# Kernel tuning notes

Hardware: AMD Instinct MI355X
Metric: run time of the kernel (lower is better)

Reference implementation:

```python
import jax, jax.numpy as jnp
import numpy as np

THRESHOLD = 0.01


def setup_inputs() -> dict:
    key = jax.random.key(0)
    kv_cache = jax.random.normal(key, (2, 16, 8192, 128), dtype=jnp.float32)
    return {"kv_cache": kv_cache}


def _dequantize_bin(kv, binmask, levels):
    # min/max restricted to the bin via +-inf sentinels (no dynamic shapes)
    inf = jnp.float32(jnp.inf)
    bmin = jnp.min(jnp.where(binmask, kv, inf))
    bmax = jnp.max(jnp.where(binmask, kv, -inf))
    has_any = jnp.any(binmask)
    valid = has_any & (bmax != bmin)
    denom = jnp.where(valid, bmax - bmin, jnp.float32(1.0))  # safe denom
    q = jnp.round((kv - bmin) / denom * levels)
    deq = q / levels * denom + bmin
    return jnp.where(binmask & valid, deq, kv)


def reference(kv_cache):
    mask = jnp.abs(kv_cache) > THRESHOLD  # large-value bin
    out = _dequantize_bin(kv_cache, ~mask, jnp.float32(15.0))   # small bin: 4-bit
    out = jnp.where(mask, _dequantize_bin(kv_cache, mask, jnp.float32(255.0)), out)  # large bin: 8-bit
    return out
```

## Files before the change

### kernel.cpp

```cpp
#include <hip/hip_runtime.h>

static constexpr float kThresh = 0.01f;
static constexpr int TPB     = 256;
static constexpr int PBLOCKS = 2048;
static constexpr int DBLOCKS = 2048;

__device__ __forceinline__ unsigned fkey(float f) {
    unsigned u = __float_as_uint(f);
    return (u & 0x80000000u) ? ~u : (u | 0x80000000u);
}
__device__ __forceinline__ float unkey(unsigned k) {
    unsigned u = (k & 0x80000000u) ? (k & 0x7fffffffu) : ~k;
    return __uint_as_float(u);
}

__device__ __forceinline__ void acc_one(float x, unsigned& smin, unsigned& smax,
                                        unsigned& lmin, unsigned& lmax) {
    unsigned k = fkey(x);
    if (fabsf(x) > kThresh) {
        lmin = min(lmin, k);
        lmax = max(lmax, k);
    } else {
        smin = min(smin, k);
        smax = max(smax, k);
    }
}

__device__ __forceinline__ void acc4(float4 v, unsigned& smin, unsigned& smax,
                                     unsigned& lmin, unsigned& lmax) {
    acc_one(v.x, smin, smax, lmin, lmax);
    acc_one(v.y, smin, smax, lmin, lmax);
    acc_one(v.z, smin, smax, lmin, lmax);
    acc_one(v.w, smin, smax, lmin, lmax);
}

__device__ __forceinline__ void wave_reduce4(unsigned& smin, unsigned& smax,
                                             unsigned& lmin, unsigned& lmax) {
    #pragma unroll
    for (int off = 32; off > 0; off >>= 1) {
        smin = min(smin, (unsigned)__shfl_down((int)smin, off));
        smax = max(smax, (unsigned)__shfl_down((int)smax, off));
        lmin = min(lmin, (unsigned)__shfl_down((int)lmin, off));
        lmax = max(lmax, (unsigned)__shfl_down((int)lmax, off));
    }
}

__device__ __forceinline__ float deq1(float x, float smin, float ssc, float sis, bool sv,
                                      float lmin, float lsc, float lis, bool lv) {
    bool large = fabsf(x) > kThresh;
    float bmin = large ? lmin : smin;
    float sc   = large ? lsc : ssc;
    float is   = large ? lis : sis;
    bool  v    = large ? lv : sv;
    float q = rintf((x - bmin) * sc);
    float d = fmaf(q, is, bmin);
    return v ? d : x;
}

__global__ __launch_bounds__(TPB) void kv_partial(const float* __restrict__ in, int n,
                                                  unsigned* __restrict__ partials) {
    unsigned smin = 0xFFFFFFFFu, smax = 0u, lmin = 0xFFFFFFFFu, lmax = 0u;
    const int n4 = n >> 2;
    const float4* __restrict__ in4 = (const float4*)in;
    const int stride = gridDim.x * TPB;
    int i = blockIdx.x * TPB + threadIdx.x;
    for (; i + 3 * stride < n4; i += 4 * stride) {
        float4 a = in4[i];
        float4 b = in4[i + stride];
        float4 c = in4[i + 2 * stride];
        float4 d = in4[i + 3 * stride];
        acc4(a, smin, smax, lmin, lmax);
        acc4(b, smin, smax, lmin, lmax);
        acc4(c, smin, smax, lmin, lmax);
        acc4(d, smin, smax, lmin, lmax);
    }
    for (; i < n4; i += stride) acc4(in4[i], smin, smax, lmin, lmax);
    for (int j = (n4 << 2) + blockIdx.x * TPB + threadIdx.x; j < n; j += stride)
        acc_one(in[j], smin, smax, lmin, lmax);

    wave_reduce4(smin, smax, lmin, lmax);

    __shared__ unsigned ls[4][4];
    const int wave = threadIdx.x >> 6;
    if ((threadIdx.x & 63) == 0) {
        ls[wave][0] = smin; ls[wave][1] = smax; ls[wave][2] = lmin; ls[wave][3] = lmax;
    }
    __syncthreads();
    if (threadIdx.x == 0) {
        unsigned a = ls[0][0], b = ls[0][1], c = ls[0][2], d = ls[0][3];
        #pragma unroll
        for (int w = 1; w < 4; ++w) {
            a = min(a, ls[w][0]); b = max(b, ls[w][1]);
            c = min(c, ls[w][2]); d = max(d, ls[w][3]);
        }
        partials[blockIdx.x * 4 + 0] = a;
        partials[blockIdx.x * 4 + 1] = b;
        partials[blockIdx.x * 4 + 2] = c;
        partials[blockIdx.x * 4 + 3] = d;
    }
}

__global__ __launch_bounds__(TPB) void kv_final(const unsigned* __restrict__ partials,
                                                unsigned* __restrict__ ws) {
    unsigned smin = 0xFFFFFFFFu, smax = 0u, lmin = 0xFFFFFFFFu, lmax = 0u;
    for (int i = threadIdx.x; i < PBLOCKS; i += TPB) {
        smin = min(smin, partials[4 * i + 0]);
        smax = max(smax, partials[4 * i + 1]);
        lmin = min(lmin, partials[4 * i + 2]);
        lmax = max(lmax, partials[4 * i + 3]);
    }
    wave_reduce4(smin, smax, lmin, lmax);

    __shared__ unsigned ls[4][4];
    const int wave = threadIdx.x >> 6;
    if ((threadIdx.x & 63) == 0) {
        ls[wave][0] = smin; ls[wave][1] = smax; ls[wave][2] = lmin; ls[wave][3] = lmax;
    }
    __syncthreads();
    if (threadIdx.x == 0) {
        unsigned a = ls[0][0], b = ls[0][1], c = ls[0][2], d = ls[0][3];
        #pragma unroll
        for (int w = 1; w < 4; ++w) {
            a = min(a, ls[w][0]); b = max(b, ls[w][1]);
            c = min(c, ls[w][2]); d = max(d, ls[w][3]);
        }
        ws[0] = a; ws[1] = b; ws[2] = c; ws[3] = d;
    }
}

__global__ __launch_bounds__(TPB) void kv_dequant(const float* __restrict__ in,
                                                  float* __restrict__ out, int n,
                                                  const unsigned* __restrict__ partials,
                                                  int pcount) {
    unsigned fa = 0xFFFFFFFFu, fb = 0u, fc = 0xFFFFFFFFu, fd = 0u;
    for (int p = threadIdx.x; p < pcount; p += TPB) {
        fa = min(fa, partials[4 * p + 0]);
        fb = max(fb, partials[4 * p + 1]);
        fc = min(fc, partials[4 * p + 2]);
        fd = max(fd, partials[4 * p + 3]);
    }
    wave_reduce4(fa, fb, fc, fd);

    __shared__ unsigned ls[4][4];
    __shared__ float sc8[8];
    const int wave = threadIdx.x >> 6;
    if ((threadIdx.x & 63) == 0) {
        ls[wave][0] = fa; ls[wave][1] = fb; ls[wave][2] = fc; ls[wave][3] = fd;
    }
    __syncthreads();
    if (threadIdx.x == 0) {
        unsigned a = ls[0][0], b = ls[0][1], c = ls[0][2], d = ls[0][3];
        #pragma unroll
        for (int w = 1; w < 4; ++w) {
            a = min(a, ls[w][0]); b = max(b, ls[w][1]);
            c = min(c, ls[w][2]); d = max(d, ls[w][3]);
        }
        bool sv = a < b;
        bool lv = c < d;
        float smn  = unkey(a);
        float sden = sv ? (unkey(b) - smn) : 1.0f;
        float lmn  = unkey(c);
        float lden = lv ? (unkey(d) - lmn) : 1.0f;
        sc8[0] = smn; sc8[1] = 15.0f / sden;  sc8[2] = sden / 15.0f;
        sc8[3] = lmn; sc8[4] = 255.0f / lden; sc8[5] = lden / 255.0f;
        sc8[6] = sv ? 1.0f : 0.0f;
        sc8[7] = lv ? 1.0f : 0.0f;
    }
    __syncthreads();
    const float smn = sc8[0], ssc = sc8[1], sis = sc8[2];
    const float lmn = sc8[3], lsc = sc8[4], lis = sc8[5];
    const bool  sv  = sc8[6] != 0.0f, lv = sc8[7] != 0.0f;

    const int n4 = n >> 2;
    const float4* __restrict__ in4 = (const float4*)in;
    float4* __restrict__ out4 = (float4*)out;
    const int stride = gridDim.x * TPB;
    int k = blockIdx.x * TPB + threadIdx.x;
    for (; k + 3 * stride < n4; k += 4 * stride) {
        float4 a = in4[k];
        float4 b = in4[k + stride];
        float4 c = in4[k + 2 * stride];
        float4 d = in4[k + 3 * stride];
        float4 ra, rb, rc, rd;
        ra.x = deq1(a.x, smn, ssc, sis, sv, lmn, lsc, lis, lv);
        ra.y = deq1(a.y, smn, ssc, sis, sv, lmn, lsc, lis, lv);
        ra.z = deq1(a.z, smn, ssc, sis, sv, lmn, lsc, lis, lv);
        ra.w = deq1(a.w, smn, ssc, sis, sv, lmn, lsc, lis, lv);
        rb.x = deq1(b.x, smn, ssc, sis, sv, lmn, lsc, lis, lv);
        rb.y = deq1(b.y, smn, ssc, sis, sv, lmn, lsc, lis, lv);
        rb.z = deq1(b.z, smn, ssc, sis, sv, lmn, lsc, lis, lv);
        rb.w = deq1(b.w, smn, ssc, sis, sv, lmn, lsc, lis, lv);
        rc.x = deq1(c.x, smn, ssc, sis, sv, lmn, lsc, lis, lv);
        rc.y = deq1(c.y, smn, ssc, sis, sv, lmn, lsc, lis, lv);
        rc.z = deq1(c.z, smn, ssc, sis, sv, lmn, lsc, lis, lv);
        rc.w = deq1(c.w, smn, ssc, sis, sv, lmn, lsc, lis, lv);
        rd.x = deq1(d.x, smn, ssc, sis, sv, lmn, lsc, lis, lv);
        rd.y = deq1(d.y, smn, ssc, sis, sv, lmn, lsc, lis, lv);
        rd.z = deq1(d.z, smn, ssc, sis, sv, lmn, lsc, lis, lv);
        rd.w = deq1(d.w, smn, ssc, sis, sv, lmn, lsc, lis, lv);
        out4[k]              = ra;
        out4[k + stride]     = rb;
        out4[k + 2 * stride] = rc;
        out4[k + 3 * stride] = rd;
    }
    for (; k < n4; k += stride) {
        float4 a = in4[k];
        float4 r;
        r.x = deq1(a.x, smn, ssc, sis, sv, lmn, lsc, lis, lv);
        r.y = deq1(a.y, smn, ssc, sis, sv, lmn, lsc, lis, lv);
        r.z = deq1(a.z, smn, ssc, sis, sv, lmn, lsc, lis, lv);
        r.w = deq1(a.w, smn, ssc, sis, sv, lmn, lsc, lis, lv);
        out4[k] = r;
    }
    for (int j = (n4 << 2) + blockIdx.x * TPB + threadIdx.x; j < n; j += stride)
        out[j] = deq1(in[j], smn, ssc, sis, sv, lmn, lsc, lis, lv);
}

extern "C" void kernel_launch(void* const* d_in, const int* in_sizes, int n_in,
                              void* d_out, int out_size, void* d_ws, size_t ws_size,
                              hipStream_t stream) {
    const float* in = (const float*)d_in[0];
    float* out = (float*)d_out;
    unsigned* ws = (unsigned*)d_ws;
    const int n = in_sizes[0];

    if (ws_size >= (size_t)(PBLOCKS * 4) * sizeof(unsigned)) {
        unsigned* pt = ws;
        kv_partial<<<PBLOCKS, TPB, 0, stream>>>(in, n, pt);
        kv_dequant<<<DBLOCKS, TPB, 0, stream>>>(in, out, n, pt, PBLOCKS);
    } else {
        unsigned* pt = (unsigned*)d_out;
        kv_partial<<<PBLOCKS, TPB, 0, stream>>>(in, n, pt);
        kv_final<<<1, TPB, 0, stream>>>(pt, ws);
        kv_dequant<<<DBLOCKS, TPB, 0, stream>>>(in, out, n, ws, 1);
    }
}
```

Measured before the change: 255.6 us.

## Fuse min/max reduction and dequant into one cooperative kernel with grid sync

Replaces the two-kernel pipeline (partial reduction, then dequant that re-reduces partials) with one cooperative kernel. It computes per-block min/max, does a grid-wide sync, reduces the partials once per block and then dequantizes. This removes a kernel launch boundary and shrinks the partial count to 1024 blocks. The cost is a grid barrier, the 1024-block limit on parallelism, and a second full read of the 64MB input that the L2/MALL is unlikely to cache. If the cooperative launch fails, the code falls back to the old path.

```diff
diff --git a/kernel.cpp b/kernel.cpp
--- a/kernel.cpp
+++ b/kernel.cpp
@@ -1,7 +1,11 @@
 #include <hip/hip_runtime.h>
+#include <hip/hip_cooperative_groups.h>
+
+namespace cg = cooperative_groups;
 
 static constexpr float kThresh = 0.01f;
 static constexpr int TPB     = 256;
+static constexpr int NBLK    = 1024;
 static constexpr int PBLOCKS = 2048;
 static constexpr int DBLOCKS = 2048;
 
@@ -55,6 +59,131 @@
     float q = rintf((x - bmin) * sc);
     float d = fmaf(q, is, bmin);
     return v ? d : x;
+}
+
+__global__ __launch_bounds__(TPB, 4) void kv_fused(const float* __restrict__ in,
+                                                   float* __restrict__ out, int n,
+                                                   unsigned* __restrict__ pt) {
+    const int n4 = n >> 2;
+    const float4* __restrict__ in4 = (const float4*)in;
+    const int tid = blockIdx.x * TPB + threadIdx.x;
+    const int stride = NBLK * TPB;
+
+    unsigned smin = 0xFFFFFFFFu, smax = 0u, lmin = 0xFFFFFFFFu, lmax = 0u;
+    int i = tid;
+    for (; i + 3 * stride < n4; i += 4 * stride) {
+        float4 a = in4[i];
+        float4 b = in4[i + stride];
+        float4 c = in4[i + 2 * stride];
+        float4 d = in4[i + 3 * stride];
+        acc4(a, smin, smax, lmin, lmax);
+        acc4(b, smin, smax, lmin, lmax);
+        acc4(c, smin, smax, lmin, lmax);
+        acc4(d, smin, smax, lmin, lmax);
+    }
+    for (; i < n4; i += stride) acc4(in4[i], smin, smax, lmin, lmax);
+    for (int j = (n4 << 2) + tid; j < n; j += stride)
+        acc_one(in[j], smin, smax, lmin, lmax);
+
+    wave_reduce4(smin, smax, lmin, lmax);
+
+    __shared__ unsigned ls[4][4];
+    __shared__ float sc8[8];
+    const int wave = threadIdx.x >> 6;
+    if ((threadIdx.x & 63) == 0) {
+        ls[wave][0] = smin; ls[wave][1] = smax; ls[wave][2] = lmin; ls[wave][3] = lmax;
+    }
+    __syncthreads();
+    if (threadIdx.x == 0) {
+        unsigned a = ls[0][0], b = ls[0][1], c = ls[0][2], d = ls[0][3];
+        #pragma unroll
+        for (int w = 1; w < 4; ++w) {
+            a = min(a, ls[w][0]); b = max(b, ls[w][1]);
+            c = min(c, ls[w][2]); d = max(d, ls[w][3]);
+        }
+        __hip_atomic_store(&pt[blockIdx.x + 0 * NBLK], a, __ATOMIC_RELAXED, __HIP_MEMORY_SCOPE_AGENT);
+        __hip_atomic_store(&pt[blockIdx.x + 1 * NBLK], b, __ATOMIC_RELAXED, __HIP_MEMORY_SCOPE_AGENT);
+        __hip_atomic_store(&pt[blockIdx.x + 2 * NBLK], c, __ATOMIC_RELAXED, __HIP_MEMORY_SCOPE_AGENT);
+        __hip_atomic_store(&pt[blockIdx.x + 3 * NBLK], d, __ATOMIC_RELAXED, __HIP_MEMORY_SCOPE_AGENT);
+    }
+
+    cg::this_grid().sync();
+
+    unsigned fa = 0xFFFFFFFFu, fb = 0u, fc = 0xFFFFFFFFu, fd = 0u;
+    for (int p = threadIdx.x; p < NBLK; p += TPB) {
+        fa = min(fa, __hip_atomic_load(&pt[p + 0 * NBLK], __ATOMIC_RELAXED, __HIP_MEMORY_SCOPE_AGENT));
+        fb = max(fb, __hip_atomic_load(&pt[p + 1 * NBLK], __ATOMIC_RELAXED, __HIP_MEMORY_SCOPE_AGENT));
+        fc = min(fc, __hip_atomic_load(&pt[p + 2 * NBLK], __ATOMIC_RELAXED, __HIP_MEMORY_SCOPE_AGENT));
+        fd = max(fd, __hip_atomic_load(&pt[p + 3 * NBLK], __ATOMIC_RELAXED, __HIP_MEMORY_SCOPE_AGENT));
+    }
+    wave_reduce4(fa, fb, fc, fd);
+    if ((threadIdx.x & 63) == 0) {
+        ls[wave][0] = fa; ls[wave][1] = fb; ls[wave][2] = fc; ls[wave][3] = fd;
+    }
+    __syncthreads();
+    if (threadIdx.x == 0) {
+        unsigned a = ls[0][0], b = ls[0][1], c = ls[0][2], d = ls[0][3];
+        #pragma unroll
+        for (int w = 1; w < 4; ++w) {
+            a = min(a, ls[w][0]); b = max(b, ls[w][1]);
+            c = min(c, ls[w][2]); d = max(d, ls[w][3]);
+        }
+        bool sv = a < b;
+        bool lv = c < d;
+        float smn  = unkey(a);
+        float sden = sv ? (unkey(b) - smn) : 1.0f;
+        float lmn  = unkey(c);
+        float lden = lv ? (unkey(d) - lmn) : 1.0f;
+        sc8[0] = smn; sc8[1] = 15.0f / sden;  sc8[2] = sden / 15.0f;
+        sc8[3] = lmn; sc8[4] = 255.0f / lden; sc8[5] = lden / 255.0f;
+        sc8[6] = sv ? 1.0f : 0.0f;
+        sc8[7] = lv ? 1.0f : 0.0f;
+    }
+    __syncthreads();
+    const float smn = sc8[0], ssc = sc8[1], sis = sc8[2];
+    const float lmn = sc8[3], lsc = sc8[4], lis = sc8[5];
+    const bool  sv  = sc8[6] != 0.0f, lv = sc8[7] != 0.0f;
+
+    float4* __restrict__ out4 = (float4*)out;
+    int k = tid;
+    for (; k + 3 * stride < n4; k += 4 * stride) {
+        float4 a = in4[k];
+        float4 b = in4[k + stride];
+        float4 c = in4[k + 2 * stride];
+        float4 d = in4[k + 3 * stride];
+        float4 ra, rb, rc, rd;
+        ra.x = deq1(a.x, smn, ssc, sis, sv, lmn, lsc, lis, lv);
+        ra.y = deq1(a.y, smn, ssc, sis, sv, lmn, lsc, lis, lv);
+        ra.z = deq1(a.z, smn, ssc, sis, sv, lmn, lsc, lis, lv);
+        ra.w = deq1(a.w, smn, ssc, sis, sv, lmn, lsc, lis, lv);
+        rb.x = deq1(b.x, smn, ssc, sis, sv, lmn, lsc, lis, lv);
+        rb.y = deq1(b.y, smn, ssc, sis, sv, lmn, lsc, lis, lv);
+        rb.z = deq1(b.z, smn, ssc, sis, sv, lmn, lsc, lis, lv);
+        rb.w = deq1(b.w, smn, ssc, sis, sv, lmn, lsc, lis, lv);
+        rc.x = deq1(c.x, smn, ssc, sis, sv, lmn, lsc, lis, lv);
+        rc.y = deq1(c.y, smn, ssc, sis, sv, lmn, lsc, lis, lv);
+        rc.z = deq1(c.z, smn, ssc, sis, sv, lmn, lsc, lis, lv);
+        rc.w = deq1(c.w, smn, ssc, sis, sv, lmn, lsc, lis, lv);
+        rd.x = deq1(d.x, smn, ssc, sis, sv, lmn, lsc, lis, lv);
+        rd.y = deq1(d.y, smn, ssc, sis, sv, lmn, lsc, lis, lv);
+        rd.z = deq1(d.z, smn, ssc, sis, sv, lmn, lsc, lis, lv);
+        rd.w = deq1(d.w, smn, ssc, sis, sv, lmn, lsc, lis, lv);
+        out4[k]              = ra;
+        out4[k + stride]     = rb;
+        out4[k + 2 * stride] = rc;
+        out4[k + 3 * stride] = rd;
+    }
+    for (; k < n4; k += stride) {
+        float4 a = in4[k];
+        float4 r;
+        r.x = deq1(a.x, smn, ssc, sis, sv, lmn, lsc, lis, lv);
+        r.y = deq1(a.y, smn, ssc, sis, sv, lmn, lsc, lis, lv);
+        r.z = deq1(a.z, smn, ssc, sis, sv, lmn, lsc, lis, lv);
+        r.w = deq1(a.w, smn, ssc, sis, sv, lmn, lsc, lis, lv);
+        out4[k] = r;
+    }
+    for (int j = (n4 << 2) + tid; j < n; j += stride)
+        out[j] = deq1(in[j], smn, ssc, sis, sv, lmn, lsc, lis, lv);
 }
 
 __global__ __launch_bounds__(TPB) void kv_partial(const float* __restrict__ in, int n,
@@ -224,6 +353,15 @@
     unsigned* ws = (unsigned*)d_ws;
     const int n = in_sizes[0];
 
+    if (ws_size >= (size_t)(4 * NBLK) * sizeof(unsigned)) {
+        unsigned* pt = ws;
+        void* args[] = { (void*)&in, (void*)&out, (void*)&n, (void*)&pt };
+        hipError_t err = hipLaunchCooperativeKernel((void*)kv_fused, dim3(NBLK), dim3(TPB),
+                                                    args, 0, stream);
+        if (err == hipSuccess) return;
+        (void)hipGetLastError();
+    }
+
     if (ws_size >= (size_t)(PBLOCKS * 4) * sizeof(unsigned)) {
         unsigned* pt = ws;
         kv_partial<<<PBLOCKS, TPB, 0, stream>>>(in, n, pt);
```

Result: slower. 388.7 us (+52.1%).
